# Optimization experiments

Measured on AMD Instinct MI355X. Metric: run time of the kernel, lower is better.

Reference implementation:

```python
import jax, jax.numpy as jnp
import numpy as np

N_NODES = 100000
N_EDGES = 1600000
N_FEAT = 16
HEADS = 4


def _feast_conv(x, src, dst, U, c, W, b):
    """FeaStConv: q = softmax_h(u^T(x_j - x_i) + c); out_i = mean_j sum_h q_h * (W_h x_j) + b."""
    n = x.shape[0]
    e = src.shape[0]
    xj = x[src]                                   # [E, Fin] gather
    q = jax.nn.softmax(jnp.matmul(xj - x[dst], U) + c, axis=-1)   # [E, H]
    xs = jnp.matmul(xj, W).reshape(e, HEADS, -1)  # [E, H, Fout]
    msg = jnp.einsum('eh,eho->eo', q, xs)         # [E, Fout]
    deg = jax.ops.segment_sum(jnp.ones((e,), x.dtype), dst, num_segments=n)
    agg = jax.ops.segment_sum(msg, dst, num_segments=n)
    return agg / jnp.maximum(deg, 1.0)[:, None] + b


def setup_inputs() -> dict:
    key = jax.random.key(0)
    ks = jax.random.split(key, 32)
    s = 0.1
    d = {
        'x': jax.random.normal(ks[0], (N_NODES, N_FEAT), jnp.float32),
        'edge_index': jax.random.randint(ks[1], (2, N_EDGES), 0, N_NODES, jnp.int32),
        # conv1: 16 -> 16
        'U1': jax.random.normal(ks[2], (N_FEAT, HEADS), jnp.float32) * s,
        'c1': jnp.zeros((HEADS,), jnp.float32),
        'W1': jax.random.normal(ks[3], (N_FEAT, HEADS * 16), jnp.float32) * s,
        'b1': jnp.zeros((16,), jnp.float32),
        # conv2: 16 -> 32
        'U2': jax.random.normal(ks[4], (16, HEADS), jnp.float32) * s,
        'c2': jnp.zeros((HEADS,), jnp.float32),
        'W2': jax.random.normal(ks[5], (16, HEADS * 32), jnp.float32) * s,
        'b2': jnp.zeros((32,), jnp.float32),
        # conv3: 32 -> 64
        'U3': jax.random.normal(ks[6], (32, HEADS), jnp.float32) * s,
        'c3': jnp.zeros((HEADS,), jnp.float32),
        'W3': jax.random.normal(ks[7], (32, HEADS * 64), jnp.float32) * s,
        'b3': jnp.zeros((64,), jnp.float32),
        # linear tail 64->32->16->8->4->1
        'lw1': jax.random.normal(ks[8], (64, 32), jnp.float32) * s,
        'lb1': jnp.zeros((32,), jnp.float32),
        'lw2': jax.random.normal(ks[9], (32, 16), jnp.float32) * s,
        'lb2': jnp.zeros((16,), jnp.float32),
        'lw3': jax.random.normal(ks[10], (16, 8), jnp.float32) * s,
        'lb3': jnp.zeros((8,), jnp.float32),
        'lw4': jax.random.normal(ks[11], (8, 4), jnp.float32) * s,
        'lb4': jnp.zeros((4,), jnp.float32),
        'lw5': jax.random.normal(ks[12], (4, 1), jnp.float32) * s,
        'lb5': jnp.zeros((1,), jnp.float32),
    }
    return d


def reference(x, edge_index, U1, c1, W1, b1, U2, c2, W2, b2, U3, c3, W3, b3,
              lw1, lb1, lw2, lb2, lw3, lb3, lw4, lb4, lw5, lb5):
    src, dst = edge_index[0], edge_index[1]
    h = jax.nn.relu(_feast_conv(x, src, dst, U1, c1, W1, b1))
    h = jax.nn.relu(_feast_conv(h, src, dst, U2, c2, W2, b2))
    h = jax.nn.relu(_feast_conv(h, src, dst, U3, c3, W3, b3))
    # dropout disabled (inference / drop_bool=False): Linear+ReLU tail
    h = jax.nn.relu(jnp.matmul(h, lw1) + lb1)
    h = jax.nn.relu(jnp.matmul(h, lw2) + lb2)
    h = jax.nn.relu(jnp.matmul(h, lw3) + lb3)
    h = jax.nn.relu(jnp.matmul(h, lw4) + lb4)
    return jax.nn.sigmoid(jnp.matmul(h, lw5) + lb5)   # [N, 1]
```

## Files before the change

### kernel.cpp

```cpp
#include <hip/hip_runtime.h>
#include <math.h>

#define N_NODES 100000
#define N_EDGES 1600000
#define HEADS 4
#define NBKT ((N_NODES + 255) / 256)
#define CHUNK_E 4096
#define NCHUNK ((N_EDGES + CHUNK_E - 1) / CHUNK_E)

typedef unsigned short ushort_t;

__device__ __forceinline__ ushort_t f2bf(float x) {
    unsigned u = __float_as_uint(x);
    u += 0x7FFF + ((u >> 16) & 1);
    return (ushort_t)(u >> 16);
}
__device__ __forceinline__ float bf2f(ushort_t v) {
    return __uint_as_float(((unsigned)v) << 16);
}
__device__ __forceinline__ void unpack2(unsigned u, float& lo, float& hi) {
    lo = __uint_as_float(u << 16);
    hi = __uint_as_float(u & 0xffff0000u);
}


__global__ void zero_int_kernel(int* __restrict__ ptr, int n) {
    int i = blockIdx.x * blockDim.x + threadIdx.x;
    if (i < n) ptr[i] = 0;
}

__global__ __launch_bounds__(256) void bhist_kernel(const int* __restrict__ dst,
                                                    int* __restrict__ bucket_cnt) {
    __shared__ int h[NBKT];
    for (int i = threadIdx.x; i < NBKT; i += 256) h[i] = 0;
    __syncthreads();
    int base = blockIdx.x * CHUNK_E;
    #pragma unroll
    for (int j = 0; j < CHUNK_E / 256; j++) {
        int e = base + j * 256 + threadIdx.x;
        if (e < N_EDGES) atomicAdd(&h[dst[e] >> 8], 1);
    }
    __syncthreads();
    for (int i = threadIdx.x; i < NBKT; i += 256)
        if (h[i]) atomicAdd(&bucket_cnt[i], h[i]);
}

__global__ __launch_bounds__(512) void bscan_kernel(const int* __restrict__ bucket_cnt,
                                                    int* __restrict__ bucket_base,
                                                    int* __restrict__ bucket_cursor) {
    __shared__ int tmp[512];
    int i = threadIdx.x;
    int v = (i < NBKT) ? bucket_cnt[i] : 0;
    tmp[i] = v;
    __syncthreads();
    for (int off = 1; off < 512; off <<= 1) {
        int t = (i >= off) ? tmp[i - off] : 0;
        __syncthreads();
        tmp[i] += t;
        __syncthreads();
    }
    int excl = tmp[i] - v;
    if (i < NBKT) { bucket_base[i] = excl; bucket_cursor[i] = excl; }
    if (i == NBKT) bucket_base[NBKT] = N_EDGES;
}

__global__ __launch_bounds__(256) void partition_kernel(const int* __restrict__ src,
                                                        const int* __restrict__ dst,
                                                        int* __restrict__ bucket_cursor,
                                                        int* __restrict__ csr_tmp) {
    constexpr int EPT = CHUNK_E / 256;
    __shared__ int h[NBKT];
    __shared__ int gbase[NBKT];
    __shared__ int rcnt[NBKT];
    for (int i = threadIdx.x; i < NBKT; i += 256) { h[i] = 0; rcnt[i] = 0; }
    __syncthreads();
    int base = blockIdx.x * CHUNK_E;
    int d[EPT], s[EPT];
    #pragma unroll
    for (int j = 0; j < EPT; j++) {
        int e = base + j * 256 + threadIdx.x;
        d[j] = (e < N_EDGES) ? dst[e] : -1;
        s[j] = (e < N_EDGES) ? src[e] : 0;
        if (d[j] >= 0) atomicAdd(&h[d[j] >> 8], 1);
    }
    __syncthreads();
    for (int i = threadIdx.x; i < NBKT; i += 256)
        if (h[i]) gbase[i] = atomicAdd(&bucket_cursor[i], h[i]);
    __syncthreads();
    #pragma unroll
    for (int j = 0; j < EPT; j++) {
        if (d[j] >= 0) {
            int b = d[j] >> 8;
            int r = atomicAdd(&rcnt[b], 1);
            csr_tmp[gbase[b] + r] = ((d[j] & 255) << 20) | s[j];
        }
    }
}

__global__ __launch_bounds__(256) void bucket_build_kernel(const int* __restrict__ bucket_base,
                                                           const int* __restrict__ csr_tmp,
                                                           int* __restrict__ rowptr,
                                                           int* __restrict__ csr_src) {
    __shared__ int cnt[256];
    __shared__ int tscan[256];
    __shared__ int exc[256];
    __shared__ int stage[8192];
    int b = blockIdx.x;
    int rbeg = bucket_base[b], rend = bucket_base[b + 1];
    int sz = rend - rbeg;
    int tid = threadIdx.x;

    cnt[tid] = 0;
    __syncthreads();
    for (int k = rbeg + tid; k < rend; k += 256) atomicAdd(&cnt[csr_tmp[k] >> 20], 1);
    __syncthreads();
    int v = cnt[tid];
    tscan[tid] = v;
    __syncthreads();
    for (int off = 1; off < 256; off <<= 1) {
        int t = (tid >= off) ? tscan[tid - off] : 0;
        __syncthreads();
        tscan[tid] += t;
        __syncthreads();
    }
    int ex = tscan[tid] - v;
    int node = b * 256 + tid;
    if (node < N_NODES) rowptr[node] = rbeg + ex;
    if (b == 0 && tid == 0) rowptr[N_NODES] = N_EDGES;
    exc[tid] = ex;
    cnt[tid] = 0;
    __syncthreads();

    if (sz <= 8192) {
        for (int k = rbeg + tid; k < rend; k += 256) {
            int pk = csr_tmp[k];
            int dl = pk >> 20;
            int r  = atomicAdd(&cnt[dl], 1);
            stage[exc[dl] + r] = pk & ((1 << 20) - 1);
        }
        __syncthreads();
        for (int i = tid; i < sz; i += 256) csr_src[rbeg + i] = stage[i];
    } else {
        for (int k = rbeg + tid; k < rend; k += 256) {
            int pk = csr_tmp[k];
            int dl = pk >> 20;
            int r  = atomicAdd(&cnt[dl], 1);
            csr_src[rbeg + exc[dl] + r] = pk & ((1 << 20) - 1);
        }
    }
}


__global__ __launch_bounds__(256) void p_cast_kernel(
        const float* __restrict__ x, const float* __restrict__ U,
        float* __restrict__ p,
        ushort_t* __restrict__ xbf)
{
    int n = blockIdx.x * blockDim.x + threadIdx.x;
    if (n >= N_NODES) return;
    float a0 = 0, a1 = 0, a2 = 0, a3 = 0;
    const float* hr = x + (size_t)n * 16;
    float xv[16];
    #pragma unroll
    for (int f = 0; f < 16; f++) {
        xv[f] = hr[f];
        a0 += xv[f] * U[f * 4 + 0];
        a1 += xv[f] * U[f * 4 + 1];
        a2 += xv[f] * U[f * 4 + 2];
        a3 += xv[f] * U[f * 4 + 3];
    }
    *(float4*)(p + (size_t)n * 4) = make_float4(a0, a1, a2, a3);
    #pragma unroll
    for (int j = 0; j < 4; j++) {
        ushort4 u;
        u.x = f2bf(xv[4 * j + 0]); u.y = f2bf(xv[4 * j + 1]);
        u.z = f2bf(xv[4 * j + 2]); u.w = f2bf(xv[4 * j + 3]);
        *(ushort4*)(xbf + (size_t)n * 16 + 4 * j) = u;
    }
}


template<int FIN>
__global__ __launch_bounds__(256) void zgather_bf16_kernel(
        const int* __restrict__ rowptr, const int* __restrict__ csr_src,
        const float* __restrict__ p, const float* __restrict__ cvec,
        const ushort_t* __restrict__ hprev,
        float* __restrict__ z)
{
    constexpr int NPB   = 256 / FIN;
    constexpr int CHUNK = 512;
    __shared__ int    sbeg[NPB + 1];
    __shared__ float4 qs[CHUNK];
    __shared__ int    ssrc[CHUNK];

    int tid  = threadIdx.x;
    int nloc = tid / FIN;
    int f    = tid - nloc * FIN;
    int n0   = blockIdx.x * NPB;
    int n    = n0 + nloc;

    if (tid <= NPB) {
        int idx = n0 + tid;
        sbeg[tid] = rowptr[idx > N_NODES ? N_NODES : idx];
    }
    float c0 = cvec[0], c1 = cvec[1], c2 = cvec[2], c3 = cvec[3];
    __syncthreads();

    int BB = sbeg[0], BE = sbeg[NPB];
    int beg = sbeg[nloc], end = sbeg[nloc + 1];
    float a0 = 0, a1 = 0, a2 = 0, a3 = 0;

    for (int cbase = BB; cbase < BE; cbase += CHUNK) {
        int cend = min(cbase + CHUNK, BE);
        __syncthreads();
        for (int k = cbase + tid; k < cend; k += 256) {
            int s = csr_src[k];
            int lo = 0, hi = NPB;
            while (hi - lo > 1) { int mid = (lo + hi) >> 1; if (k < sbeg[mid]) hi = mid; else lo = mid; }
            float4 ps = *(const float4*)(p + (size_t)s * 4);
            float4 pd = *(const float4*)(p + (size_t)(n0 + lo) * 4);
            float l0 = ps.x - pd.x + c0;
            float l1 = ps.y - pd.y + c1;
            float l2 = ps.z - pd.z + c2;
            float l3 = ps.w - pd.w + c3;
            float m  = fmaxf(fmaxf(l0, l1), fmaxf(l2, l3));
            float e0 = __expf(l0 - m), e1 = __expf(l1 - m);
            float e2 = __expf(l2 - m), e3 = __expf(l3 - m);
            float deg = (float)(sbeg[lo + 1] - sbeg[lo]);
            float inv = 1.0f / (fmaxf(deg, 1.0f) * (e0 + e1 + e2 + e3));
            qs[k - cbase]   = make_float4(e0 * inv, e1 * inv, e2 * inv, e3 * inv);
            ssrc[k - cbase] = s;
        }
        __syncthreads();
        int kb = (beg > cbase ? beg : cbase) - cbase;
        int ke = (end < cend ? end : cend) - cbase;
        int k = kb;
        for (; k + 8 <= ke; k += 8) {
            ushort_t u[8];
            #pragma unroll
            for (int j = 0; j < 8; j++)
                u[j] = hprev[(size_t)ssrc[k + j] * FIN + f];
            #pragma unroll
            for (int j = 0; j < 8; j++) {
                float xv = bf2f(u[j]);
                float4 q = qs[k + j];
                a0 += q.x * xv; a1 += q.y * xv; a2 += q.z * xv; a3 += q.w * xv;
            }
        }
        for (; k + 4 <= ke; k += 4) {
            ushort_t u[4];
            #pragma unroll
            for (int j = 0; j < 4; j++)
                u[j] = hprev[(size_t)ssrc[k + j] * FIN + f];
            #pragma unroll
            for (int j = 0; j < 4; j++) {
                float xv = bf2f(u[j]);
                float4 q = qs[k + j];
                a0 += q.x * xv; a1 += q.y * xv; a2 += q.z * xv; a3 += q.w * xv;
            }
        }
        for (; k < ke; k++) {
            float xv = bf2f(hprev[(size_t)ssrc[k] * FIN + f]);
            float4 q = qs[k];
            a0 += q.x * xv; a1 += q.y * xv; a2 += q.z * xv; a3 += q.w * xv;
        }
    }

    if (n < N_NODES) {
        size_t base = (size_t)n * (4 * FIN) + f;
        z[base]           = a0;
        z[base + FIN]     = a1;
        z[base + 2 * FIN] = a2;
        z[base + 3 * FIN] = a3;
    }
}


template<int FIN, int FOUT, int MODE>
__global__ __launch_bounds__(256, 4) void post_kernel(
        const float* __restrict__ z,
        const float* __restrict__ W,
        const float* __restrict__ b,
        ushort_t* __restrict__ out_bf,
        const float* __restrict__ Unext,
        float* __restrict__ pnext)
{
    constexpr int K   = 4 * FIN;
    constexpr int OL  = FOUT / 4;
    constexpr int NPB = 4 * (256 / OL);
    constexpr int WSZ = FIN * 4 * FOUT;
    constexpr bool PNEXT = (MODE == 2);
    __shared__ float Wp[WSZ];
    __shared__ float htile[PNEXT ? NPB * FOUT : 1];
    __shared__ float Uloc[PNEXT ? FOUT * 4 : 1];
    for (int i = threadIdx.x; i < WSZ; i += 256) {
        int f = i / (4 * FOUT);
        int r = i - f * (4 * FOUT);
        int h = r / FOUT;
        int o = r - h * FOUT;
        Wp[(h * FIN + f) * FOUT + o] = W[i];
    }
    if (PNEXT) {
        for (int i = threadIdx.x; i < FOUT * 4; i += 256) Uloc[i] = Unext[i];
    }
    __syncthreads();

    int ol = threadIdx.x % OL;
    int g  = threadIdx.x / OL;
    int n0 = blockIdx.x * NPB + g * 4;

    float4 bv = *(const float4*)(b + 4 * ol);
    float4 acc[4];
    const float* zr[4];
    #pragma unroll
    for (int j = 0; j < 4; j++) {
        acc[j] = make_float4(0.f, 0.f, 0.f, 0.f);
        int nn = n0 + j; if (nn > N_NODES - 1) nn = N_NODES - 1;
        zr[j] = z + (size_t)nn * K;
    }

    #pragma unroll 2
    for (int kq = 0; kq < K / 4; kq++) {
        float4 zv[4];
        #pragma unroll
        for (int j = 0; j < 4; j++)
            zv[j] = *(const float4*)(zr[j] + 4 * kq);
        #pragma unroll
        for (int jj = 0; jj < 4; jj++) {
            float4 wv = *(const float4*)(Wp + (4 * kq + jj) * FOUT + 4 * ol);
            #pragma unroll
            for (int j = 0; j < 4; j++) {
                float s = (&zv[j].x)[jj];
                acc[j].x += s * wv.x;
                acc[j].y += s * wv.y;
                acc[j].z += s * wv.z;
                acc[j].w += s * wv.w;
            }
        }
    }

    #pragma unroll
    for (int j = 0; j < 4; j++) {
        int nn = n0 + j;
        float4 r;
        r.x = fmaxf(acc[j].x + bv.x, 0.0f);
        r.y = fmaxf(acc[j].y + bv.y, 0.0f);
        r.z = fmaxf(acc[j].z + bv.z, 0.0f);
        r.w = fmaxf(acc[j].w + bv.w, 0.0f);
        if (PNEXT)
            *(float4*)(htile + (g * 4 + j) * FOUT + 4 * ol) = r;
        if (nn < N_NODES) {
            ushort4 u;
            u.x = f2bf(r.x); u.y = f2bf(r.y); u.z = f2bf(r.z); u.w = f2bf(r.w);
            *(ushort4*)(out_bf + (size_t)nn * FOUT + 4 * ol) = u;
        }
    }

    if (PNEXT) {
        __syncthreads();
        int tid = threadIdx.x;
        if (tid < NPB) {
            int nn = blockIdx.x * NPB + tid;
            if (nn < N_NODES) {
                float a0 = 0, a1 = 0, a2 = 0, a3 = 0;
                const float* hr = htile + tid * FOUT;
                #pragma unroll
                for (int f = 0; f < FOUT; f++) {
                    float xv = hr[f];
                    a0 += xv * Uloc[f * 4 + 0];
                    a1 += xv * Uloc[f * 4 + 1];
                    a2 += xv * Uloc[f * 4 + 2];
                    a3 += xv * Uloc[f * 4 + 3];
                }
                *(float4*)(pnext + (size_t)nn * 4) = make_float4(a0, a1, a2, a3);
            }
        }
    }
}


__global__ __launch_bounds__(256) void tail_kernel(
        const ushort_t* __restrict__ h,
        const float* __restrict__ lw1, const float* __restrict__ lb1,
        const float* __restrict__ lw2, const float* __restrict__ lb2,
        const float* __restrict__ lw3, const float* __restrict__ lb3,
        const float* __restrict__ lw4, const float* __restrict__ lb4,
        const float* __restrict__ lw5, const float* __restrict__ lb5,
        float* __restrict__ out)
{
    __shared__ float w1[64 * 32], w2[32 * 16], w3[16 * 8], w4[8 * 4], w5[4];
    __shared__ float B1[32], B2[16], B3[8], B4[4], B5[1];
    for (int i = threadIdx.x; i < 64 * 32; i += blockDim.x) w1[i] = lw1[i];
    for (int i = threadIdx.x; i < 32 * 16; i += blockDim.x) w2[i] = lw2[i];
    for (int i = threadIdx.x; i < 16 * 8;  i += blockDim.x) w3[i] = lw3[i];
    for (int i = threadIdx.x; i < 8 * 4;   i += blockDim.x) w4[i] = lw4[i];
    for (int i = threadIdx.x; i < 4;       i += blockDim.x) w5[i] = lw5[i];
    for (int i = threadIdx.x; i < 32; i += blockDim.x) B1[i] = lb1[i];
    for (int i = threadIdx.x; i < 16; i += blockDim.x) B2[i] = lb2[i];
    for (int i = threadIdx.x; i < 8;  i += blockDim.x) B3[i] = lb3[i];
    for (int i = threadIdx.x; i < 4;  i += blockDim.x) B4[i] = lb4[i];
    if (threadIdx.x == 0) B5[0] = lb5[0];
    __syncthreads();

    int n = blockIdx.x * blockDim.x + threadIdx.x;
    if (n >= N_NODES) return;

    float a[64];
    const uint4* hrow = (const uint4*)(h + (size_t)n * 64);
    #pragma unroll
    for (int j = 0; j < 8; j++) {
        uint4 v = hrow[j];
        unpack2(v.x, a[8 * j + 0], a[8 * j + 1]);
        unpack2(v.y, a[8 * j + 2], a[8 * j + 3]);
        unpack2(v.z, a[8 * j + 4], a[8 * j + 5]);
        unpack2(v.w, a[8 * j + 6], a[8 * j + 7]);
    }

    float t1[32];
    for (int o = 0; o < 32; o++) {
        float acc = B1[o];
        #pragma unroll
        for (int i = 0; i < 64; i++) acc += a[i] * w1[i * 32 + o];
        t1[o] = fmaxf(acc, 0.0f);
    }
    float t2[16];
    for (int o = 0; o < 16; o++) {
        float acc = B2[o];
        #pragma unroll
        for (int i = 0; i < 32; i++) acc += t1[i] * w2[i * 16 + o];
        t2[o] = fmaxf(acc, 0.0f);
    }
    float t3[8];
    for (int o = 0; o < 8; o++) {
        float acc = B3[o];
        #pragma unroll
        for (int i = 0; i < 16; i++) acc += t2[i] * w3[i * 8 + o];
        t3[o] = fmaxf(acc, 0.0f);
    }
    float t4[4];
    for (int o = 0; o < 4; o++) {
        float acc = B4[o];
        #pragma unroll
        for (int i = 0; i < 8; i++) acc += t3[i] * w4[i * 4 + o];
        t4[o] = fmaxf(acc, 0.0f);
    }
    float zf = B5[0];
    #pragma unroll
    for (int i = 0; i < 4; i++) zf += t4[i] * w5[i];
    out[n] = 1.0f / (1.0f + expf(-zf));
}


extern "C" void kernel_launch(void* const* d_in, const int* in_sizes, int n_in,
                              void* d_out, int out_size, void* d_ws, size_t ws_size,
                              hipStream_t stream) {
    const float* x   = (const float*)d_in[0];
    const int*   ei  = (const int*)d_in[1];
    const int*   src = ei;
    const int*   dst = ei + N_EDGES;
    const float* U1 = (const float*)d_in[2];  const float* c1 = (const float*)d_in[3];
    const float* W1 = (const float*)d_in[4];  const float* b1 = (const float*)d_in[5];
    const float* U2 = (const float*)d_in[6];  const float* c2 = (const float*)d_in[7];
    const float* W2 = (const float*)d_in[8];  const float* b2 = (const float*)d_in[9];
    const float* U3 = (const float*)d_in[10]; const float* c3 = (const float*)d_in[11];
    const float* W3 = (const float*)d_in[12]; const float* b3 = (const float*)d_in[13];
    const float* lw1 = (const float*)d_in[14]; const float* lb1 = (const float*)d_in[15];
    const float* lw2 = (const float*)d_in[16]; const float* lb2 = (const float*)d_in[17];
    const float* lw3 = (const float*)d_in[18]; const float* lb3 = (const float*)d_in[19];
    const float* lw4 = (const float*)d_in[20]; const float* lb4 = (const float*)d_in[21];
    const float* lw5 = (const float*)d_in[22]; const float* lb5 = (const float*)d_in[23];

    char* ws = (char*)d_ws;
    size_t off = 0;
    auto alloc = [&](size_t bytes) -> void* {
        void* ptr = (void*)(ws + off);
        off += (bytes + 255) & ~(size_t)255;
        return ptr;
    };
    int*      bucket_cnt    = (int*)alloc((size_t)(NBKT + 1) * 4);
    int*      bucket_base   = (int*)alloc((size_t)(NBKT + 1) * 4);
    int*      bucket_cursor = (int*)alloc((size_t)NBKT * 4);
    int*      csr_tmp       = (int*)alloc((size_t)N_EDGES * 4);
    int*      rowptr        = (int*)alloc(((size_t)N_NODES + 1) * 4);
    int*      csr_src       = (int*)alloc((size_t)N_EDGES * 4);
    float*    p             = (float*)alloc((size_t)N_NODES * 4 * 4);
    float*    z             = (float*)alloc((size_t)N_NODES * 128 * 4);
    ushort_t* xbf           = (ushort_t*)alloc((size_t)N_NODES * 16 * 2);
    ushort_t* h1bf          = (ushort_t*)alloc((size_t)N_NODES * 16 * 2);
    ushort_t* h2bf          = (ushort_t*)alloc((size_t)N_NODES * 32 * 2);
    ushort_t* h3bf          = (ushort_t*)alloc((size_t)N_NODES * 64 * 2);
    (void)ws_size;

    const int B = 256;
    int gN = (N_NODES + B - 1) / B;

    zero_int_kernel<<<(NBKT + 255) / 256, B, 0, stream>>>(bucket_cnt, NBKT);
    bhist_kernel<<<NCHUNK, B, 0, stream>>>(dst, bucket_cnt);
    bscan_kernel<<<1, 512, 0, stream>>>(bucket_cnt, bucket_base, bucket_cursor);
    partition_kernel<<<NCHUNK, B, 0, stream>>>(src, dst, bucket_cursor, csr_tmp);
    bucket_build_kernel<<<NBKT, B, 0, stream>>>(bucket_base, csr_tmp, rowptr, csr_src);

    const int ZG16 = (N_NODES + (256 / 16) - 1) / (256 / 16);
    const int ZG32 = (N_NODES + (256 / 32) - 1) / (256 / 32);
    const int NPB1 = 4 * (256 / (16 / 4));
    const int NPB2 = 4 * (256 / (32 / 4));
    const int NPB3 = 4 * (256 / (64 / 4));

    p_cast_kernel<<<gN, B, 0, stream>>>(x, U1, p, xbf);
    zgather_bf16_kernel<16><<<ZG16, B, 0, stream>>>(rowptr, csr_src, p, c1, xbf, z);
    post_kernel<16, 16, 2><<<(N_NODES + NPB1 - 1) / NPB1, B, 0, stream>>>(
        z, W1, b1, h1bf, U2, p);

    zgather_bf16_kernel<16><<<ZG16, B, 0, stream>>>(rowptr, csr_src, p, c2, h1bf, z);
    post_kernel<16, 32, 2><<<(N_NODES + NPB2 - 1) / NPB2, B, 0, stream>>>(
        z, W2, b2, h2bf, U3, p);

    zgather_bf16_kernel<32><<<ZG32, B, 0, stream>>>(rowptr, csr_src, p, c3, h2bf, z);
    post_kernel<32, 64, 3><<<(N_NODES + NPB3 - 1) / NPB3, B, 0, stream>>>(
        z, W3, b3, h3bf, nullptr, nullptr);

    tail_kernel<<<gN, B, 0, stream>>>(h3bf, lw1, lb1, lw2, lb2, lw3, lb3,
                                      lw4, lb4, lw5, lb5, (float*)d_out);
}
```

Before: 346.3 us.

## Fuse edge gather and per-node head projection into one conv kernel

Merges the z-gather kernel and the post (W-projection, bias, ReLU, next-layer attention projection) kernel into one kernel per FeaStConv layer. The per-node z rows now stay in a shared-memory tile that reuses the gather staging buffer, so the large intermediate z array no longer makes a round trip through global memory, and three kernel launches go away. In exchange, the projection reads W directly from global memory with strided scalar loads and gives up the previous float4 register blocking. The kernel also overwrites p, which it gathers from, while other blocks may still be reading it, so there is a risk of a cross-block race.

```diff
diff --git a/kernel.cpp b/kernel.cpp
--- a/kernel.cpp
+++ b/kernel.cpp
@@ -180,18 +180,26 @@
 }
 
 
-template<int FIN>
-__global__ __launch_bounds__(256) void zgather_bf16_kernel(
+template<int FIN, int FOUT, int MODE>
+__global__ __launch_bounds__(256) void conv_fused_kernel(
         const int* __restrict__ rowptr, const int* __restrict__ csr_src,
         const float* __restrict__ p, const float* __restrict__ cvec,
         const ushort_t* __restrict__ hprev,
-        float* __restrict__ z)
+        const float* __restrict__ W,
+        const float* __restrict__ b,
+        ushort_t* __restrict__ out_bf,
+        const float* __restrict__ Unext,
+        float* __restrict__ pnext)
 {
     constexpr int NPB   = 256 / FIN;
     constexpr int CHUNK = 512;
-    __shared__ int    sbeg[NPB + 1];
-    __shared__ float4 qs[CHUNK];
-    __shared__ int    ssrc[CHUNK];
+    constexpr int K     = 4 * FIN;
+    __shared__ int sbeg[NPB + 1];
+    __shared__ __align__(16) char ubuf[CHUNK * 16 + CHUNK * 4];
+    float4* qs   = (float4*)ubuf;
+    int*    ssrc = (int*)(ubuf + CHUNK * 16);
+    float*  ztile = (float*)ubuf;
+    float*  hout  = (float*)(ubuf + NPB * K * 4);
 
     int tid  = threadIdx.x;
     int nloc = tid / FIN;
@@ -266,113 +274,56 @@
         }
     }
 
-    if (n < N_NODES) {
-        size_t base = (size_t)n * (4 * FIN) + f;
-        z[base]           = a0;
-        z[base + FIN]     = a1;
-        z[base + 2 * FIN] = a2;
-        z[base + 3 * FIN] = a3;
-    }
-}
-
-
-template<int FIN, int FOUT, int MODE>
-__global__ __launch_bounds__(256, 4) void post_kernel(
-        const float* __restrict__ z,
-        const float* __restrict__ W,
-        const float* __restrict__ b,
-        ushort_t* __restrict__ out_bf,
-        const float* __restrict__ Unext,
-        float* __restrict__ pnext)
-{
-    constexpr int K   = 4 * FIN;
-    constexpr int OL  = FOUT / 4;
-    constexpr int NPB = 4 * (256 / OL);
-    constexpr int WSZ = FIN * 4 * FOUT;
-    constexpr bool PNEXT = (MODE == 2);
-    __shared__ float Wp[WSZ];
-    __shared__ float htile[PNEXT ? NPB * FOUT : 1];
-    __shared__ float Uloc[PNEXT ? FOUT * 4 : 1];
-    for (int i = threadIdx.x; i < WSZ; i += 256) {
-        int f = i / (4 * FOUT);
-        int r = i - f * (4 * FOUT);
-        int h = r / FOUT;
-        int o = r - h * FOUT;
-        Wp[(h * FIN + f) * FOUT + o] = W[i];
-    }
-    if (PNEXT) {
-        for (int i = threadIdx.x; i < FOUT * 4; i += 256) Uloc[i] = Unext[i];
-    }
-    __syncthreads();
-
-    int ol = threadIdx.x % OL;
-    int g  = threadIdx.x / OL;
-    int n0 = blockIdx.x * NPB + g * 4;
-
-    float4 bv = *(const float4*)(b + 4 * ol);
-    float4 acc[4];
-    const float* zr[4];
-    #pragma unroll
-    for (int j = 0; j < 4; j++) {
-        acc[j] = make_float4(0.f, 0.f, 0.f, 0.f);
-        int nn = n0 + j; if (nn > N_NODES - 1) nn = N_NODES - 1;
-        zr[j] = z + (size_t)nn * K;
-    }
-
-    #pragma unroll 2
-    for (int kq = 0; kq < K / 4; kq++) {
-        float4 zv[4];
-        #pragma unroll
-        for (int j = 0; j < 4; j++)
-            zv[j] = *(const float4*)(zr[j] + 4 * kq);
-        #pragma unroll
-        for (int jj = 0; jj < 4; jj++) {
-            float4 wv = *(const float4*)(Wp + (4 * kq + jj) * FOUT + 4 * ol);
-            #pragma unroll
-            for (int j = 0; j < 4; j++) {
-                float s = (&zv[j].x)[jj];
-                acc[j].x += s * wv.x;
-                acc[j].y += s * wv.y;
-                acc[j].z += s * wv.z;
-                acc[j].w += s * wv.w;
+    __syncthreads();
+    {
+        float* zr = ztile + nloc * K + f;
+        zr[0]        = a0;
+        zr[FIN]      = a1;
+        zr[2 * FIN]  = a2;
+        zr[3 * FIN]  = a3;
+    }
+    __syncthreads();
+
+    constexpr int OPT = (NPB * FOUT) / 256;
+    #pragma unroll
+    for (int r = 0; r < OPT; r++) {
+        int i = tid + 256 * r;
+        int j = i / FOUT;
+        int o = i - j * FOUT;
+        const float* zr = ztile + j * K;
+        const float* Wc = W + o;
+        float ac0 = 0, ac1 = 0, ac2 = 0, ac3 = 0;
+        for (int h = 0; h < 4; h++) {
+            #pragma unroll 2
+            for (int f4 = 0; f4 < FIN; f4 += 4) {
+                ac0 += zr[h * FIN + f4 + 0] * Wc[(size_t)(f4 + 0) * 4 * FOUT + h * FOUT];
+                ac1 += zr[h * FIN + f4 + 1] * Wc[(size_t)(f4 + 1) * 4 * FOUT + h * FOUT];
+                ac2 += zr[h * FIN + f4 + 2] * Wc[(size_t)(f4 + 2) * 4 * FOUT + h * FOUT];
+                ac3 += zr[h * FIN + f4 + 3] * Wc[(size_t)(f4 + 3) * 4 * FOUT + h * FOUT];
             }
         }
-    }
-
-    #pragma unroll
-    for (int j = 0; j < 4; j++) {
+        float res = fmaxf((ac0 + ac1) + (ac2 + ac3) + b[o], 0.0f);
+        if (MODE == 2) hout[j * FOUT + o] = res;
         int nn = n0 + j;
-        float4 r;
-        r.x = fmaxf(acc[j].x + bv.x, 0.0f);
-        r.y = fmaxf(acc[j].y + bv.y, 0.0f);
-        r.z = fmaxf(acc[j].z + bv.z, 0.0f);
-        r.w = fmaxf(acc[j].w + bv.w, 0.0f);
-        if (PNEXT)
-            *(float4*)(htile + (g * 4 + j) * FOUT + 4 * ol) = r;
-        if (nn < N_NODES) {
-            ushort4 u;
-            u.x = f2bf(r.x); u.y = f2bf(r.y); u.z = f2bf(r.z); u.w = f2bf(r.w);
-            *(ushort4*)(out_bf + (size_t)nn * FOUT + 4 * ol) = u;
-        }
-    }
-
-    if (PNEXT) {
-        __syncthreads();
-        int tid = threadIdx.x;
+        if (nn < N_NODES) out_bf[(size_t)nn * FOUT + o] = f2bf(res);
+    }
+
+    if (MODE == 2) {
+        __syncthreads();
         if (tid < NPB) {
-            int nn = blockIdx.x * NPB + tid;
+            int nn = n0 + tid;
             if (nn < N_NODES) {
-                float a0 = 0, a1 = 0, a2 = 0, a3 = 0;
-                const float* hr = htile + tid * FOUT;
+                float b0 = 0, b1 = 0, b2 = 0, b3 = 0;
+                const float* hr = hout + tid * FOUT;
                 #pragma unroll
-                for (int f = 0; f < FOUT; f++) {
-                    float xv = hr[f];
-                    a0 += xv * Uloc[f * 4 + 0];
-                    a1 += xv * Uloc[f * 4 + 1];
-                    a2 += xv * Uloc[f * 4 + 2];
-                    a3 += xv * Uloc[f * 4 + 3];
+                for (int ff = 0; ff < FOUT; ff++) {
+                    float xv = hr[ff];
+                    b0 += xv * Unext[ff * 4 + 0];
+                    b1 += xv * Unext[ff * 4 + 1];
+                    b2 += xv * Unext[ff * 4 + 2];
+                    b3 += xv * Unext[ff * 4 + 3];
                 }
-                *(float4*)(pnext + (size_t)nn * 4) = make_float4(a0, a1, a2, a3);
+                *(float4*)(pnext + (size_t)nn * 4) = make_float4(b0, b1, b2, b3);
             }
         }
     }
@@ -484,7 +435,6 @@
     int*      rowptr        = (int*)alloc(((size_t)N_NODES + 1) * 4);
     int*      csr_src       = (int*)alloc((size_t)N_EDGES * 4);
     float*    p             = (float*)alloc((size_t)N_NODES * 4 * 4);
-    float*    z             = (float*)alloc((size_t)N_NODES * 128 * 4);
     ushort_t* xbf           = (ushort_t*)alloc((size_t)N_NODES * 16 * 2);
     ushort_t* h1bf          = (ushort_t*)alloc((size_t)N_NODES * 16 * 2);
     ushort_t* h2bf          = (ushort_t*)alloc((size_t)N_NODES * 32 * 2);
@@ -502,22 +452,16 @@
 
     const int ZG16 = (N_NODES + (256 / 16) - 1) / (256 / 16);
     const int ZG32 = (N_NODES + (256 / 32) - 1) / (256 / 32);
-    const int NPB1 = 4 * (256 / (16 / 4));
-    const int NPB2 = 4 * (256 / (32 / 4));
-    const int NPB3 = 4 * (256 / (64 / 4));
 
     p_cast_kernel<<<gN, B, 0, stream>>>(x, U1, p, xbf);
-    zgather_bf16_kernel<16><<<ZG16, B, 0, stream>>>(rowptr, csr_src, p, c1, xbf, z);
-    post_kernel<16, 16, 2><<<(N_NODES + NPB1 - 1) / NPB1, B, 0, stream>>>(
-        z, W1, b1, h1bf, U2, p);
-
-    zgather_bf16_kernel<16><<<ZG16, B, 0, stream>>>(rowptr, csr_src, p, c2, h1bf, z);
-    post_kernel<16, 32, 2><<<(N_NODES + NPB2 - 1) / NPB2, B, 0, stream>>>(
-        z, W2, b2, h2bf, U3, p);
-
-    zgather_bf16_kernel<32><<<ZG32, B, 0, stream>>>(rowptr, csr_src, p, c3, h2bf, z);
-    post_kernel<32, 64, 3><<<(N_NODES + NPB3 - 1) / NPB3, B, 0, stream>>>(
-        z, W3, b3, h3bf, nullptr, nullptr);
+    conv_fused_kernel<16, 16, 2><<<ZG16, B, 0, stream>>>(
+        rowptr, csr_src, p, c1, xbf, W1, b1, h1bf, U2, p);
+
+    conv_fused_kernel<16, 32, 2><<<ZG16, B, 0, stream>>>(
+        rowptr, csr_src, p, c2, h1bf, W2, b2, h2bf, U3, p);
+
+    conv_fused_kernel<32, 64, 3><<<ZG32, B, 0, stream>>>(
+        rowptr, csr_src, p, c3, h2bf, W3, b3, h3bf, nullptr, nullptr);
 
     tail_kernel<<<gN, B, 0, stream>>>(h3bf, lw1, lb1, lw2, lb2, lw3, lb3,
                                       lw4, lb4, lw5, lb5, (float*)d_out);
```

Measured after the change: 397.1 us. +14.7%, slower.

## Fuse edge histogram with node cast kernel and drop global histogram atomics

Applied to the files above, without the earlier changes.

Merges the bucket histogram pass and the per-node projection/bf16 cast into one launch, with blocks split by index between the two jobs. Each histogram block writes its own row of counts instead of atomically adding into a shared global array, which also removes the zeroing kernel. The single-block scan now reduces all per-chunk rows per bucket itself, adding serial memory reads to that one block in exchange for fewer launches and no global atomics.

```diff
diff --git a/kernel.cpp b/kernel.cpp
--- a/kernel.cpp
+++ b/kernel.cpp
@@ -7,6 +7,7 @@
 #define NBKT ((N_NODES + 255) / 256)
 #define CHUNK_E 4096
 #define NCHUNK ((N_EDGES + CHUNK_E - 1) / CHUNK_E)
+#define GN ((N_NODES + 255) / 256)
 
 typedef unsigned short ushort_t;
 
@@ -24,33 +25,58 @@
 }
 
 
-__global__ void zero_int_kernel(int* __restrict__ ptr, int n) {
-    int i = blockIdx.x * blockDim.x + threadIdx.x;
-    if (i < n) ptr[i] = 0;
-}
-
-__global__ __launch_bounds__(256) void bhist_kernel(const int* __restrict__ dst,
-                                                    int* __restrict__ bucket_cnt) {
+__global__ __launch_bounds__(256) void bhist_pcast_kernel(
+        const int* __restrict__ dst, int* __restrict__ hist_rows,
+        const float* __restrict__ x, const float* __restrict__ U,
+        float* __restrict__ p, ushort_t* __restrict__ xbf)
+{
     __shared__ int h[NBKT];
-    for (int i = threadIdx.x; i < NBKT; i += 256) h[i] = 0;
-    __syncthreads();
-    int base = blockIdx.x * CHUNK_E;
-    #pragma unroll
-    for (int j = 0; j < CHUNK_E / 256; j++) {
-        int e = base + j * 256 + threadIdx.x;
-        if (e < N_EDGES) atomicAdd(&h[dst[e] >> 8], 1);
-    }
-    __syncthreads();
-    for (int i = threadIdx.x; i < NBKT; i += 256)
-        if (h[i]) atomicAdd(&bucket_cnt[i], h[i]);
-}
-
-__global__ __launch_bounds__(512) void bscan_kernel(const int* __restrict__ bucket_cnt,
+    if (blockIdx.x < NCHUNK) {
+        for (int i = threadIdx.x; i < NBKT; i += 256) h[i] = 0;
+        __syncthreads();
+        int base = blockIdx.x * CHUNK_E;
+        #pragma unroll
+        for (int j = 0; j < CHUNK_E / 256; j++) {
+            int e = base + j * 256 + threadIdx.x;
+            if (e < N_EDGES) atomicAdd(&h[dst[e] >> 8], 1);
+        }
+        __syncthreads();
+        for (int i = threadIdx.x; i < NBKT; i += 256)
+            hist_rows[(size_t)blockIdx.x * NBKT + i] = h[i];
+    } else {
+        int n = (blockIdx.x - NCHUNK) * 256 + threadIdx.x;
+        if (n >= N_NODES) return;
+        float a0 = 0, a1 = 0, a2 = 0, a3 = 0;
+        const float* hr = x + (size_t)n * 16;
+        float xv[16];
+        #pragma unroll
+        for (int f = 0; f < 16; f++) {
+            xv[f] = hr[f];
+            a0 += xv[f] * U[f * 4 + 0];
+            a1 += xv[f] * U[f * 4 + 1];
+            a2 += xv[f] * U[f * 4 + 2];
+            a3 += xv[f] * U[f * 4 + 3];
+        }
+        *(float4*)(p + (size_t)n * 4) = make_float4(a0, a1, a2, a3);
+        #pragma unroll
+        for (int j = 0; j < 4; j++) {
+            ushort4 u;
+            u.x = f2bf(xv[4 * j + 0]); u.y = f2bf(xv[4 * j + 1]);
+            u.z = f2bf(xv[4 * j + 2]); u.w = f2bf(xv[4 * j + 3]);
+            *(ushort4*)(xbf + (size_t)n * 16 + 4 * j) = u;
+        }
+    }
+}
+
+
+__global__ __launch_bounds__(512) void bscan_kernel(const int* __restrict__ hist_rows,
                                                     int* __restrict__ bucket_base,
                                                     int* __restrict__ bucket_cursor) {
     __shared__ int tmp[512];
     int i = threadIdx.x;
-    int v = (i < NBKT) ? bucket_cnt[i] : 0;
+    int v = 0;
+    if (i < NBKT)
+        for (int r = 0; r < NCHUNK; r++) v += hist_rows[(size_t)r * NBKT + i];
     tmp[i] = v;
     __syncthreads();
     for (int off = 1; off < 512; off <<= 1) {
@@ -63,6 +89,7 @@
     if (i < NBKT) { bucket_base[i] = excl; bucket_cursor[i] = excl; }
     if (i == NBKT) bucket_base[NBKT] = N_EDGES;
 }
+
 
 __global__ __launch_bounds__(256) void partition_kernel(const int* __restrict__ src,
                                                         const int* __restrict__ dst,
@@ -96,6 +123,7 @@
         }
     }
 }
+
 
 __global__ __launch_bounds__(256) void bucket_build_kernel(const int* __restrict__ bucket_base,
                                                            const int* __restrict__ csr_tmp,
@@ -147,35 +175,6 @@
             int r  = atomicAdd(&cnt[dl], 1);
             csr_src[rbeg + exc[dl] + r] = pk & ((1 << 20) - 1);
         }
-    }
-}
-
-
-__global__ __launch_bounds__(256) void p_cast_kernel(
-        const float* __restrict__ x, const float* __restrict__ U,
-        float* __restrict__ p,
-        ushort_t* __restrict__ xbf)
-{
-    int n = blockIdx.x * blockDim.x + threadIdx.x;
-    if (n >= N_NODES) return;
-    float a0 = 0, a1 = 0, a2 = 0, a3 = 0;
-    const float* hr = x + (size_t)n * 16;
-    float xv[16];
-    #pragma unroll
-    for (int f = 0; f < 16; f++) {
-        xv[f] = hr[f];
-        a0 += xv[f] * U[f * 4 + 0];
-        a1 += xv[f] * U[f * 4 + 1];
-        a2 += xv[f] * U[f * 4 + 2];
-        a3 += xv[f] * U[f * 4 + 3];
-    }
-    *(float4*)(p + (size_t)n * 4) = make_float4(a0, a1, a2, a3);
-    #pragma unroll
-    for (int j = 0; j < 4; j++) {
-        ushort4 u;
-        u.x = f2bf(xv[4 * j + 0]); u.y = f2bf(xv[4 * j + 1]);
-        u.z = f2bf(xv[4 * j + 2]); u.w = f2bf(xv[4 * j + 3]);
-        *(ushort4*)(xbf + (size_t)n * 16 + 4 * j) = u;
     }
 }
 
@@ -477,7 +476,7 @@
         off += (bytes + 255) & ~(size_t)255;
         return ptr;
     };
-    int*      bucket_cnt    = (int*)alloc((size_t)(NBKT + 1) * 4);
+    int*      hist_rows     = (int*)alloc((size_t)NCHUNK * NBKT * 4);
     int*      bucket_base   = (int*)alloc((size_t)(NBKT + 1) * 4);
     int*      bucket_cursor = (int*)alloc((size_t)NBKT * 4);
     int*      csr_tmp       = (int*)alloc((size_t)N_EDGES * 4);
@@ -492,11 +491,10 @@
     (void)ws_size;
 
     const int B = 256;
-    int gN = (N_NODES + B - 1) / B;
-
-    zero_int_kernel<<<(NBKT + 255) / 256, B, 0, stream>>>(bucket_cnt, NBKT);
-    bhist_kernel<<<NCHUNK, B, 0, stream>>>(dst, bucket_cnt);
-    bscan_kernel<<<1, 512, 0, stream>>>(bucket_cnt, bucket_base, bucket_cursor);
+    int gN = GN;
+
+    bhist_pcast_kernel<<<NCHUNK + GN, B, 0, stream>>>(dst, hist_rows, x, U1, p, xbf);
+    bscan_kernel<<<1, 512, 0, stream>>>(hist_rows, bucket_base, bucket_cursor);
     partition_kernel<<<NCHUNK, B, 0, stream>>>(src, dst, bucket_cursor, csr_tmp);
     bucket_build_kernel<<<NBKT, B, 0, stream>>>(bucket_base, csr_tmp, rowptr, csr_src);
 
@@ -506,7 +504,6 @@
     const int NPB2 = 4 * (256 / (32 / 4));
     const int NPB3 = 4 * (256 / (64 / 4));
 
-    p_cast_kernel<<<gN, B, 0, stream>>>(x, U1, p, xbf);
     zgather_bf16_kernel<16><<<ZG16, B, 0, stream>>>(rowptr, csr_src, p, c1, xbf, z);
     post_kernel<16, 16, 2><<<(N_NODES + NPB1 - 1) / NPB1, B, 0, stream>>>(
         z, W1, b1, h1bf, U2, p);
```

Result: no change. 352.0 us (+1.6%).
